# Kernel optimization log

Measured on AMD Instinct MI355X. Metric: run time of the kernel, lower is better.

## Reference

```python
import jax, jax.numpy as jnp
import numpy as np

CUTOFF = 8.0
NUM_G = 50
HID = 128
NUM_INTER = 3
NUM_NODES = 50000
NUM_EDGES = 1600000
NUM_GRAPHS = 128
MAX_Z = 100
LOG2 = float(np.log(2.0))


def ssp(x):
    # PyG ShiftedSoftplus
    return jax.nn.softplus(x) - LOG2


def setup_inputs() -> dict:
    key = jax.random.key(0)
    ks = jax.random.split(key, 20)
    s = 0.1
    pos = jax.random.normal(ks[0], (NUM_NODES, 3), dtype=jnp.float32) * 4.0
    edge_shift = jax.random.normal(ks[1], (NUM_EDGES, 3), dtype=jnp.float32) * 0.5
    z = jax.random.randint(ks[2], (NUM_NODES,), 0, MAX_Z, dtype=jnp.int32)
    edge_index = jax.random.randint(ks[3], (2, NUM_EDGES), 0, NUM_NODES, dtype=jnp.int32)
    batch = jnp.sort(jax.random.randint(ks[4], (NUM_NODES,), 0, NUM_GRAPHS, dtype=jnp.int32))
    emb = jax.random.normal(ks[5], (MAX_Z, HID), dtype=jnp.float32) * s
    mlp_w1 = jax.random.normal(ks[6], (NUM_INTER, NUM_G, HID), dtype=jnp.float32) * s
    mlp_b1 = jnp.zeros((NUM_INTER, HID), jnp.float32)
    mlp_w2 = jax.random.normal(ks[7], (NUM_INTER, HID, HID), dtype=jnp.float32) * s
    mlp_b2 = jnp.zeros((NUM_INTER, HID), jnp.float32)
    cf_w1 = jax.random.normal(ks[8], (NUM_INTER, HID, HID), dtype=jnp.float32) * s  # no bias (PyG lin1)
    cf_w2 = jax.random.normal(ks[9], (NUM_INTER, HID, HID), dtype=jnp.float32) * s
    cf_b2 = jnp.zeros((NUM_INTER, HID), jnp.float32)
    lin_w = jax.random.normal(ks[10], (NUM_INTER, HID, HID), dtype=jnp.float32) * s
    lin_b = jnp.zeros((NUM_INTER, HID), jnp.float32)
    head_w1 = jax.random.normal(ks[11], (HID, HID // 2), dtype=jnp.float32) * s
    head_b1 = jnp.zeros((HID // 2,), jnp.float32)
    head_w2 = jax.random.normal(ks[12], (HID // 2, 1), dtype=jnp.float32) * s
    head_b2 = jnp.zeros((1,), jnp.float32)
    return dict(pos=pos, edge_shift=edge_shift, emb=emb, mlp_w1=mlp_w1, mlp_b1=mlp_b1,
                mlp_w2=mlp_w2, mlp_b2=mlp_b2, cf_w1=cf_w1, cf_w2=cf_w2, cf_b2=cf_b2,
                lin_w=lin_w, lin_b=lin_b, head_w1=head_w1, head_b1=head_b1,
                head_w2=head_w2, head_b2=head_b2, z=z, edge_index=edge_index, batch=batch)


def reference(pos, edge_shift, emb, mlp_w1, mlp_b1, mlp_w2, mlp_b2, cf_w1, cf_w2, cf_b2,
              lin_w, lin_b, head_w1, head_b1, head_w2, head_b2, z, edge_index, batch):
    src, dst = edge_index[0], edge_index[1]
    # edge distances: pos[row] - (pos[col] + shift)
    rel = pos[src] - (pos[dst] + edge_shift)            # [E,3]
    w = jnp.linalg.norm(rel, axis=-1)                   # [E]
    # Gaussian smearing
    offset = jnp.linspace(0.0, CUTOFF, NUM_G, dtype=pos.dtype)
    coeff = -0.5 / (offset[1] - offset[0]) ** 2
    edge_attr = jnp.exp(coeff * (w[:, None] - offset) ** 2)   # [E,50]
    # cosine cutoff
    C = 0.5 * (jnp.cos(w * jnp.pi / CUTOFF) + 1.0)            # [E]
    h = emb[z]                                                # [N,128]
    for i in range(NUM_INTER):
        Wf = (ssp(edge_attr @ mlp_w1[i] + mlp_b1[i]) @ mlp_w2[i] + mlp_b2[i]) * C[:, None]  # [E,128]
        msg = (h @ cf_w1[i])[src] * Wf                   # gather-multiply  [E,128]
        agg = jax.ops.segment_sum(msg, dst, num_segments=NUM_NODES)         # scatter-sum [N,128]
        h = h + (ssp(agg @ cf_w2[i] + cf_b2[i]) @ lin_w[i] + lin_b[i])
    out_atom = ssp(h @ head_w1 + head_b1) @ head_w2 + head_b2               # [N,1]
    sums = jax.ops.segment_sum(out_atom, batch, num_segments=NUM_GRAPHS)    # [G,1]
    counts = jax.ops.segment_sum(jnp.ones((NUM_NODES, 1), out_atom.dtype), batch, num_segments=NUM_GRAPHS)
    return sums / jnp.maximum(counts, 1.0)  # mean readout; out_proj is Identity (128==128)
```

## Files before the change

kernel.cpp:

```cpp
#include <hip/hip_runtime.h>
#include <hip/hip_fp16.h>
#include <math.h>

#define NNODES  50000
#define NEDGES  1600000
#define NGRAPHS 128
#define HID     128
#define NG      50
#define NITER   3
#define TPTS    2048
#define WMAX    12.0f
#define PI_F    3.14159265358979323846f

__device__ __forceinline__ float ssp(float x) {
    float sp = fmaxf(x, 0.0f) + log1pf(expf(-fabsf(x)));
    return sp - 0.69314718055994530942f;
}

__global__ __launch_bounds__(256) void k_init_h(const float* __restrict__ emb,
                                                const int* __restrict__ z,
                                                float* __restrict__ h)
{
    int idx = blockIdx.x * 256 + threadIdx.x;
    int n = idx >> 7, c = idx & 127;
    h[idx] = emb[(z[n] << 7) + c];
}

__global__ __launch_bounds__(128) void k_table(const float* __restrict__ W1,
                                               const float* __restrict__ B1,
                                               const float* __restrict__ W2,
                                               const float* __restrict__ B2,
                                               float* __restrict__ table)
{
    int it = blockIdx.x / TPTS;
    int pt = blockIdx.x - it * TPTS;
    const float* W1i = W1 + (size_t)it * NG * HID;
    const float* B1i = B1 + (size_t)it * HID;
    const float* W2i = W2 + (size_t)it * HID * HID;
    const float* B2i = B2 + (size_t)it * HID;

    float w = pt * (WMAX / (float)(TPTS - 1));
    __shared__ float sEA[NG];
    __shared__ float sT1[HID];
    int k = threadIdx.x;
    if (k < NG) {
        float dx = 8.0f / 49.0f;
        float coeff = -0.5f / (dx * dx);
        float diff = w - (float)k * dx;
        sEA[k] = expf(coeff * diff * diff);
    }
    __syncthreads();
    float acc = B1i[k];
    for (int g = 0; g < NG; ++g) acc = fmaf(sEA[g], W1i[g * HID + k], acc);
    sT1[k] = ssp(acc);
    __syncthreads();
    float acc2 = B2i[k];
    for (int j = 0; j < HID; ++j) acc2 = fmaf(sT1[j], W2i[j * HID + k], acc2);
    table[(size_t)blockIdx.x * HID + k] = acc2;
}

__global__ __launch_bounds__(256) void k_tdelta(const float* __restrict__ raw,
                                                __half* __restrict__ ti)
{
    int idx = blockIdx.x * 256 + threadIdx.x;
    int c = idx & 127;
    int pt_it = idx >> 7;
    int pt = pt_it & (TPTS - 1);
    float v = raw[idx];
    float nv = (pt == TPTS - 1) ? v : raw[idx + HID];
    ti[(size_t)pt_it * 256 + c * 2]     = __float2half(v);
    ti[(size_t)pt_it * 256 + c * 2 + 1] = __float2half(nv - v);
}

__global__ __launch_bounds__(256) void k_hist(const int* __restrict__ ei,
                                              int* __restrict__ deg)
{
    int e = blockIdx.x * 256 + threadIdx.x;
    if (e >= NEDGES) return;
    atomicAdd(&deg[ei[NEDGES + e]], 1);
}

#define SCAN_T 1024
#define CHUNK  49
__global__ __launch_bounds__(SCAN_T) void k_scan(const int* __restrict__ deg,
                                                 int* __restrict__ rowptr,
                                                 int* __restrict__ cursor)
{
    int tid = threadIdx.x;
    int base = tid * CHUNK;
    int vals[CHUNK];
    int local = 0;
    #pragma unroll
    for (int i = 0; i < CHUNK; ++i) {
        int idx = base + i;
        int v = (idx < NNODES) ? deg[idx] : 0;
        vals[i] = local;
        local += v;
    }
    int lane = tid & 63, wid = tid >> 6;
    int x = local;
    #pragma unroll
    for (int off = 1; off < 64; off <<= 1) {
        int y = __shfl_up(x, off);
        if (lane >= off) x += y;
    }
    __shared__ int wsum[16];
    __shared__ int woff[17];
    if (lane == 63) wsum[wid] = x;
    __syncthreads();
    if (tid == 0) {
        int acc = 0;
        #pragma unroll
        for (int i = 0; i < 16; ++i) { woff[i] = acc; acc += wsum[i]; }
        woff[16] = acc;
    }
    __syncthreads();
    int threadExcl = woff[wid] + x - local;
    #pragma unroll
    for (int i = 0; i < CHUNK; ++i) {
        int idx = base + i;
        if (idx < NNODES) {
            int p = threadExcl + vals[i];
            rowptr[idx] = p;
            cursor[idx] = p;
        }
    }
    if (tid == SCAN_T - 1) rowptr[NNODES] = woff[16];
}

__global__ __launch_bounds__(256) void k_scatter(const int* __restrict__ ei,
                                                 const float* __restrict__ pos,
                                                 const float* __restrict__ shift,
                                                 int* __restrict__ cursor,
                                                 float2* __restrict__ rec)
{
    int e = blockIdx.x * 256 + threadIdx.x;
    if (e >= NEDGES) return;
    int s = ei[e], d = ei[NEDGES + e];
    float rx = pos[3*s+0] - (pos[3*d+0] + shift[3*e+0]);
    float ry = pos[3*s+1] - (pos[3*d+1] + shift[3*e+1]);
    float rz = pos[3*s+2] - (pos[3*d+2] + shift[3*e+2]);
    float w = sqrtf(rx*rx + ry*ry + rz*rz);
    int slot = atomicAdd(&cursor[d], 1);
    rec[slot] = make_float2(__int_as_float(s), w);
}

__device__ __forceinline__ void edge_contrib(float2 r, int lane,
                                             const __half2* __restrict__ hfH,
                                             const __half* __restrict__ tableH,
                                             float& ax, float& ay)
{
    int   s = __float_as_int(r.x);
    float w = r.y;
    const float SCALE = (float)(TPTS - 1) / WMAX;
    float t = fminf(w * SCALE, (float)(TPTS - 1));
    int i0 = (int)t; if (i0 > TPTS - 2) i0 = TPTS - 2;
    float fr = t - (float)i0;
    float C = 0.5f * (__cosf(w * (PI_F / 8.0f)) + 1.0f);
    uint2 tv = *((const uint2*)(tableH + (size_t)i0 * 256) + lane);
    __half2 hv = hfH[(size_t)s * 64 + lane];
    float2 p0 = __half22float2(*(__half2*)&tv.x);
    float2 p1 = __half22float2(*(__half2*)&tv.y);
    float2 hf2 = __half22float2(hv);
    ax = fmaf(fmaf(fr, p0.y, p0.x) * C, hf2.x, ax);
    ay = fmaf(fmaf(fr, p1.y, p1.x) * C, hf2.y, ay);
}

__global__ __launch_bounds__(256) void k_gather(const float2* __restrict__ rec,
                                                const int* __restrict__ rowptr,
                                                const __half2* __restrict__ hfH,
                                                const __half* __restrict__ tableH,
                                                float* __restrict__ agg)
{
    int node = blockIdx.x * 4 + (threadIdx.x >> 6);
    int lane = threadIdx.x & 63;
    int beg = rowptr[node], end = rowptr[node + 1];
    float ax0 = 0.f, ay0 = 0.f, ax1 = 0.f, ay1 = 0.f;
    int k = beg;
    for (; k + 4 <= end; k += 4) {
        float2 r0 = rec[k];
        float2 r1 = rec[k + 1];
        float2 r2 = rec[k + 2];
        float2 r3 = rec[k + 3];
        edge_contrib(r0, lane, hfH, tableH, ax0, ay0);
        edge_contrib(r1, lane, hfH, tableH, ax1, ay1);
        edge_contrib(r2, lane, hfH, tableH, ax0, ay0);
        edge_contrib(r3, lane, hfH, tableH, ax1, ay1);
    }
    for (; k < end; ++k) {
        float2 r0 = rec[k];
        edge_contrib(r0, lane, hfH, tableH, ax0, ay0);
    }
    *(float2*)(agg + (size_t)node * HID + lane * 2) = make_float2(ax0 + ax1, ay0 + ay1);
}

__global__ __launch_bounds__(512) void k_node_gemm(const float* __restrict__ A,
                                                   const float* __restrict__ W,
                                                   __half* __restrict__ outH)
{
    __shared__ float sA[128 * 132];
    int r0 = blockIdx.x * 128;
    int tid = threadIdx.x;
    for (int idx = tid; idx < 128 * 32; idx += 512) {
        int r = idx >> 5, c4 = idx & 31;
        int row = r0 + r;
        float4 v = make_float4(0.f, 0.f, 0.f, 0.f);
        if (row < NNODES) v = *(const float4*)(A + (size_t)row * HID + c4 * 4);
        *(float4*)(&sA[r * 132 + c4 * 4]) = v;
    }
    __syncthreads();
    int tx = tid & 15, ty = tid >> 4;
    int cc = tx * 8, ee = ty * 4;
    float acc[4][8];
    #pragma unroll
    for (int e = 0; e < 4; ++e)
        #pragma unroll
        for (int c = 0; c < 8; ++c) acc[e][c] = 0.f;
    for (int j = 0; j < HID; ++j) {
        float a[4];
        #pragma unroll
        for (int e = 0; e < 4; ++e) a[e] = sA[(ee + e) * 132 + j];
        float4 w0 = *(const float4*)(W + (size_t)j * HID + cc);
        float4 w1 = *(const float4*)(W + (size_t)j * HID + cc + 4);
        float wv[8] = {w0.x,w0.y,w0.z,w0.w,w1.x,w1.y,w1.z,w1.w};
        #pragma unroll
        for (int e = 0; e < 4; ++e)
            #pragma unroll
            for (int c = 0; c < 8; ++c)
                acc[e][c] = fmaf(a[e], wv[c], acc[e][c]);
    }
    #pragma unroll
    for (int e = 0; e < 4; ++e) {
        int row = r0 + ee + e;
        if (row < NNODES) {
            __half2 p0 = __floats2half2_rn(acc[e][0], acc[e][1]);
            __half2 p1 = __floats2half2_rn(acc[e][2], acc[e][3]);
            __half2 p2 = __floats2half2_rn(acc[e][4], acc[e][5]);
            __half2 p3 = __floats2half2_rn(acc[e][6], acc[e][7]);
            uint4 pk;
            pk.x = *(unsigned*)&p0; pk.y = *(unsigned*)&p1;
            pk.z = *(unsigned*)&p2; pk.w = *(unsigned*)&p3;
            *(uint4*)(outH + (size_t)row * HID + cc) = pk;
        }
    }
}

__global__ __launch_bounds__(512) void k_node_update(const float* __restrict__ agg,
                                                     const float* __restrict__ W,
                                                     const float* __restrict__ B,
                                                     const float* __restrict__ L,
                                                     const float* __restrict__ LB,
                                                     float* __restrict__ h)
{
    __shared__ float sA[128 * 132];
    int r0 = blockIdx.x * 128;
    int tid = threadIdx.x;
    for (int idx = tid; idx < 128 * 32; idx += 512) {
        int r = idx >> 5, c4 = idx & 31;
        int row = r0 + r;
        float4 v = make_float4(0.f, 0.f, 0.f, 0.f);
        if (row < NNODES) v = *(const float4*)(agg + (size_t)row * HID + c4 * 4);
        *(float4*)(&sA[r * 132 + c4 * 4]) = v;
    }
    __syncthreads();
    int tx = tid & 15, ty = tid >> 4;
    int cc = tx * 8, ee = ty * 4;
    float acc[4][8];
    {
        float4 b0 = *(const float4*)(B + cc);
        float4 b1 = *(const float4*)(B + cc + 4);
        #pragma unroll
        for (int e = 0; e < 4; ++e) {
            acc[e][0]=b0.x; acc[e][1]=b0.y; acc[e][2]=b0.z; acc[e][3]=b0.w;
            acc[e][4]=b1.x; acc[e][5]=b1.y; acc[e][6]=b1.z; acc[e][7]=b1.w;
        }
    }
    for (int j = 0; j < HID; ++j) {
        float a[4];
        #pragma unroll
        for (int e = 0; e < 4; ++e) a[e] = sA[(ee + e) * 132 + j];
        float4 w0 = *(const float4*)(W + (size_t)j * HID + cc);
        float4 w1 = *(const float4*)(W + (size_t)j * HID + cc + 4);
        float wv[8] = {w0.x,w0.y,w0.z,w0.w,w1.x,w1.y,w1.z,w1.w};
        #pragma unroll
        for (int e = 0; e < 4; ++e)
            #pragma unroll
            for (int c = 0; c < 8; ++c)
                acc[e][c] = fmaf(a[e], wv[c], acc[e][c]);
    }
    __syncthreads();
    #pragma unroll
    for (int e = 0; e < 4; ++e)
        #pragma unroll
        for (int c = 0; c < 8; ++c)
            sA[(ee + e) * 132 + cc + c] = ssp(acc[e][c]);
    __syncthreads();
    float acc2[4][8];
    {
        float4 b0 = *(const float4*)(LB + cc);
        float4 b1 = *(const float4*)(LB + cc + 4);
        #pragma unroll
        for (int e = 0; e < 4; ++e) {
            acc2[e][0]=b0.x; acc2[e][1]=b0.y; acc2[e][2]=b0.z; acc2[e][3]=b0.w;
            acc2[e][4]=b1.x; acc2[e][5]=b1.y; acc2[e][6]=b1.z; acc2[e][7]=b1.w;
        }
    }
    for (int j = 0; j < HID; ++j) {
        float a[4];
        #pragma unroll
        for (int e = 0; e < 4; ++e) a[e] = sA[(ee + e) * 132 + j];
        float4 w0 = *(const float4*)(L + (size_t)j * HID + cc);
        float4 w1 = *(const float4*)(L + (size_t)j * HID + cc + 4);
        float wv[8] = {w0.x,w0.y,w0.z,w0.w,w1.x,w1.y,w1.z,w1.w};
        #pragma unroll
        for (int e = 0; e < 4; ++e)
            #pragma unroll
            for (int c = 0; c < 8; ++c)
                acc2[e][c] = fmaf(a[e], wv[c], acc2[e][c]);
    }
    #pragma unroll
    for (int e = 0; e < 4; ++e) {
        int row = r0 + ee + e;
        if (row < NNODES) {
            float4* hp0 = (float4*)(h + (size_t)row * HID + cc);
            float4* hp1 = (float4*)(h + (size_t)row * HID + cc + 4);
            float4 h0 = *hp0, h1 = *hp1;
            h0.x += acc2[e][0]; h0.y += acc2[e][1]; h0.z += acc2[e][2]; h0.w += acc2[e][3];
            h1.x += acc2[e][4]; h1.y += acc2[e][5]; h1.z += acc2[e][6]; h1.w += acc2[e][7];
            *hp0 = h0; *hp1 = h1;
        }
    }
}

__global__ __launch_bounds__(512) void k_head(const float* __restrict__ h,
                                              const float* __restrict__ w1,
                                              const float* __restrict__ b1,
                                              const float* __restrict__ w2,
                                              const float* __restrict__ b2,
                                              const int* __restrict__ batch,
                                              float* __restrict__ sums_pad)
{
    __shared__ float sA[128 * 132];
    int r0 = blockIdx.x * 128;
    int tid = threadIdx.x;
    for (int idx = tid; idx < 128 * 32; idx += 512) {
        int r = idx >> 5, c4 = idx & 31;
        int row = r0 + r;
        float4 v = make_float4(0.f, 0.f, 0.f, 0.f);
        if (row < NNODES) v = *(const float4*)(h + (size_t)row * HID + c4 * 4);
        *(float4*)(&sA[r * 132 + c4 * 4]) = v;
    }
    __syncthreads();
    int tx = tid & 7, ty = tid >> 3;
    int cc = tx * 8, ee = ty * 2;
    float acc[2][8];
    {
        float4 b0 = *(const float4*)(b1 + cc);
        float4 bb = *(const float4*)(b1 + cc + 4);
        #pragma unroll
        for (int e = 0; e < 2; ++e) {
            acc[e][0]=b0.x; acc[e][1]=b0.y; acc[e][2]=b0.z; acc[e][3]=b0.w;
            acc[e][4]=bb.x; acc[e][5]=bb.y; acc[e][6]=bb.z; acc[e][7]=bb.w;
        }
    }
    #pragma unroll 4
    for (int j = 0; j < HID; ++j) {
        float a0 = sA[(ee + 0) * 132 + j];
        float a1 = sA[(ee + 1) * 132 + j];
        float4 w0 = *(const float4*)(w1 + (size_t)j * 64 + cc);
        float4 wv1 = *(const float4*)(w1 + (size_t)j * 64 + cc + 4);
        float wv[8] = {w0.x,w0.y,w0.z,w0.w,wv1.x,wv1.y,wv1.z,wv1.w};
        #pragma unroll
        for (int c = 0; c < 8; ++c) {
            acc[0][c] = fmaf(a0, wv[c], acc[0][c]);
            acc[1][c] = fmaf(a1, wv[c], acc[1][c]);
        }
    }
    float4 w2a = *(const float4*)(w2 + cc);
    float4 w2b = *(const float4*)(w2 + cc + 4);
    float w2v[8] = {w2a.x,w2a.y,w2a.z,w2a.w,w2b.x,w2b.y,w2b.z,w2b.w};
    float bias2 = b2[0];
    #pragma unroll
    for (int e = 0; e < 2; ++e) {
        float part = 0.f;
        #pragma unroll
        for (int c = 0; c < 8; ++c) part = fmaf(ssp(acc[e][c]), w2v[c], part);
        part += __shfl_down(part, 4, 8);
        part += __shfl_down(part, 2, 8);
        part += __shfl_down(part, 1, 8);
        if (tx == 0) {
            int row = r0 + ee + e;
            if (row < NNODES) {
                int b = batch[row];
                atomicAdd(&sums_pad[b * 16], part + bias2);
            }
        }
    }
}

__global__ void k_final(const float* __restrict__ sums_pad,
                        const int* __restrict__ batch,
                        float* __restrict__ out)
{
    int g = threadIdx.x;
    if (g >= NGRAPHS) return;
    int lo = 0, hi = NNODES;
    while (lo < hi) { int mid = (lo + hi) >> 1; if (batch[mid] < g) lo = mid + 1; else hi = mid; }
    int a = lo;
    lo = 0; hi = NNODES;
    while (lo < hi) { int mid = (lo + hi) >> 1; if (batch[mid] < g + 1) lo = mid + 1; else hi = mid; }
    float cnt = (float)(lo - a);
    out[g] = sums_pad[g * 16] / fmaxf(cnt, 1.0f);
}

extern "C" void kernel_launch(void* const* d_in, const int* in_sizes, int n_in,
                              void* d_out, int out_size, void* d_ws, size_t ws_size,
                              hipStream_t stream)
{
    const float* pos     = (const float*)d_in[0];
    const float* shift   = (const float*)d_in[1];
    const float* emb     = (const float*)d_in[2];
    const float* mlp_w1  = (const float*)d_in[3];
    const float* mlp_b1  = (const float*)d_in[4];
    const float* mlp_w2  = (const float*)d_in[5];
    const float* mlp_b2  = (const float*)d_in[6];
    const float* cf_w1   = (const float*)d_in[7];
    const float* cf_w2   = (const float*)d_in[8];
    const float* cf_b2   = (const float*)d_in[9];
    const float* lin_w   = (const float*)d_in[10];
    const float* lin_b   = (const float*)d_in[11];
    const float* head_w1 = (const float*)d_in[12];
    const float* head_b1 = (const float*)d_in[13];
    const float* head_w2 = (const float*)d_in[14];
    const float* head_b2 = (const float*)d_in[15];
    const int*   z       = (const int*)d_in[16];
    const int*   ei      = (const int*)d_in[17];
    const int*   batch   = (const int*)d_in[18];
    float* out = (float*)d_out;

    float* ws = (float*)d_ws;
    size_t off = 0;
    float*  h       = ws + off; off += (size_t)NNODES * HID;
    __half* hfH     = (__half*)(ws + off); off += (size_t)(NNODES + 48) * HID / 2;
    float*  agg     = ws + off; off += (size_t)NNODES * HID;
    float*  rawT    = ws + off; off += (size_t)3 * TPTS * HID;
    __half* tableH  = (__half*)(ws + off); off += (size_t)3 * TPTS * HID;
    float2* rec     = (float2*)(ws + off); off += (size_t)2 * NEDGES;
    int*    rowptr  = (int*)(ws + off); off += NNODES + 1;
    int*    deg     = (int*)(ws + off); off += NNODES;
    int*    cursor  = (int*)(ws + off); off += NNODES;
    float*  sums_pad= ws + off; off += NGRAPHS * 16;

    hipMemsetAsync(deg, 0, NNODES * sizeof(int), stream);
    hipMemsetAsync(sums_pad, 0, NGRAPHS * 16 * sizeof(float), stream);

    k_hist<<<(NEDGES + 255) / 256, 256, 0, stream>>>(ei, deg);
    k_scan<<<1, SCAN_T, 0, stream>>>(deg, rowptr, cursor);
    k_scatter<<<(NEDGES + 255) / 256, 256, 0, stream>>>(ei, pos, shift, cursor, rec);

    k_init_h<<<NNODES * HID / 256, 256, 0, stream>>>(emb, z, h);
    k_table<<<3 * TPTS, 128, 0, stream>>>(mlp_w1, mlp_b1, mlp_w2, mlp_b2, rawT);
    k_tdelta<<<(3 * TPTS * HID) / 256, 256, 0, stream>>>(rawT, tableH);

    int gblk = (NNODES + 127) / 128;
    for (int i = 0; i < NITER; ++i) {
        k_node_gemm<<<gblk, 512, 0, stream>>>(h, cf_w1 + (size_t)i * HID * HID, hfH);
        k_gather<<<NNODES / 4, 256, 0, stream>>>(rec, rowptr, (const __half2*)hfH,
                                                 tableH + (size_t)i * TPTS * HID * 2, agg);
        k_node_update<<<gblk, 512, 0, stream>>>(agg, cf_w2 + (size_t)i * HID * HID,
                                                cf_b2 + (size_t)i * HID,
                                                lin_w + (size_t)i * HID * HID,
                                                lin_b + (size_t)i * HID, h);
    }
    k_head<<<gblk, 512, 0, stream>>>(h, head_w1, head_b1, head_w2, head_b2, batch, sums_pad);
    k_final<<<1, 128, 0, stream>>>(sums_pad, batch, out);
}
```

Baseline: 1.077 ms.

## Move node GEMMs to fp16 MFMA with pre-transposed half weights

Replaces the fp32 SIMT tiled node GEMMs, both the cf_w1 projection and the fused cf_w2/ssp/lin update, with MFMA 16x16x16 fp16 kernels. Weights are transposed once into fp16, and h is kept in a second fp16 copy that the update kernel writes. The gather now stores agg as fp16, halving its write and read traffic. The intermediate ssp activations go through a swizzled LDS tile. This lowers the precision of the GEMM inputs and agg to fp16 and adds small setup kernels.

```diff
diff --git a/kernel.cpp b/kernel.cpp
--- a/kernel.cpp
+++ b/kernel.cpp
@@ -12,6 +12,9 @@
 #define WMAX    12.0f
 #define PI_F    3.14159265358979323846f
 
+typedef __attribute__((ext_vector_type(4))) _Float16 half4;
+typedef __attribute__((ext_vector_type(4))) float   f32x4;
+
 __device__ __forceinline__ float ssp(float x) {
     float sp = fmaxf(x, 0.0f) + log1pf(expf(-fabsf(x)));
     return sp - 0.69314718055994530942f;
@@ -19,11 +22,21 @@
 
 __global__ __launch_bounds__(256) void k_init_h(const float* __restrict__ emb,
                                                 const int* __restrict__ z,
-                                                float* __restrict__ h)
+                                                float* __restrict__ h,
+                                                _Float16* __restrict__ hH)
 {
     int idx = blockIdx.x * 256 + threadIdx.x;
     int n = idx >> 7, c = idx & 127;
-    h[idx] = emb[(z[n] << 7) + c];
+    float v = emb[(z[n] << 7) + c];
+    h[idx] = v;
+    hH[idx] = (_Float16)v;
+}
+
+__global__ __launch_bounds__(128) void k_wt(const float* __restrict__ in,
+                                            _Float16* __restrict__ out)
+{
+    int it = blockIdx.x >> 7, c = blockIdx.x & 127, j = threadIdx.x;
+    out[(size_t)it * 16384 + c * 128 + j] = (_Float16)in[(size_t)it * 16384 + j * 128 + c];
 }
 
 __global__ __launch_bounds__(128) void k_table(const float* __restrict__ W1,
@@ -170,7 +183,7 @@
                                                 const int* __restrict__ rowptr,
                                                 const __half2* __restrict__ hfH,
                                                 const __half* __restrict__ tableH,
-                                                float* __restrict__ agg)
+                                                __half2* __restrict__ aggH)
 {
     int node = blockIdx.x * 4 + (threadIdx.x >> 6);
     int lane = threadIdx.x & 63;
@@ -191,143 +204,106 @@
         float2 r0 = rec[k];
         edge_contrib(r0, lane, hfH, tableH, ax0, ay0);
     }
-    *(float2*)(agg + (size_t)node * HID + lane * 2) = make_float2(ax0 + ax1, ay0 + ay1);
-}
-
-__global__ __launch_bounds__(512) void k_node_gemm(const float* __restrict__ A,
-                                                   const float* __restrict__ W,
-                                                   __half* __restrict__ outH)
-{
-    __shared__ float sA[128 * 132];
-    int r0 = blockIdx.x * 128;
+    aggH[(size_t)node * 64 + lane] = __floats2half2_rn(ax0 + ax1, ay0 + ay1);
+}
+
+__global__ __launch_bounds__(256) void k_ngemm_mfma(const _Float16* __restrict__ hH,
+                                                    const _Float16* __restrict__ Wt,
+                                                    _Float16* __restrict__ outH)
+{
     int tid = threadIdx.x;
-    for (int idx = tid; idx < 128 * 32; idx += 512) {
-        int r = idx >> 5, c4 = idx & 31;
-        int row = r0 + r;
-        float4 v = make_float4(0.f, 0.f, 0.f, 0.f);
-        if (row < NNODES) v = *(const float4*)(A + (size_t)row * HID + c4 * 4);
-        *(float4*)(&sA[r * 132 + c4 * 4]) = v;
-    }
-    __syncthreads();
-    int tx = tid & 15, ty = tid >> 4;
-    int cc = tx * 8, ee = ty * 4;
-    float acc[4][8];
-    #pragma unroll
-    for (int e = 0; e < 4; ++e)
-        #pragma unroll
-        for (int c = 0; c < 8; ++c) acc[e][c] = 0.f;
-    for (int j = 0; j < HID; ++j) {
-        float a[4];
-        #pragma unroll
-        for (int e = 0; e < 4; ++e) a[e] = sA[(ee + e) * 132 + j];
-        float4 w0 = *(const float4*)(W + (size_t)j * HID + cc);
-        float4 w1 = *(const float4*)(W + (size_t)j * HID + cc + 4);
-        float wv[8] = {w0.x,w0.y,w0.z,w0.w,w1.x,w1.y,w1.z,w1.w};
-        #pragma unroll
-        for (int e = 0; e < 4; ++e)
-            #pragma unroll
-            for (int c = 0; c < 8; ++c)
-                acc[e][c] = fmaf(a[e], wv[c], acc[e][c]);
-    }
-    #pragma unroll
-    for (int e = 0; e < 4; ++e) {
-        int row = r0 + ee + e;
-        if (row < NNODES) {
-            __half2 p0 = __floats2half2_rn(acc[e][0], acc[e][1]);
-            __half2 p1 = __floats2half2_rn(acc[e][2], acc[e][3]);
-            __half2 p2 = __floats2half2_rn(acc[e][4], acc[e][5]);
-            __half2 p3 = __floats2half2_rn(acc[e][6], acc[e][7]);
-            uint4 pk;
-            pk.x = *(unsigned*)&p0; pk.y = *(unsigned*)&p1;
-            pk.z = *(unsigned*)&p2; pk.w = *(unsigned*)&p3;
-            *(uint4*)(outH + (size_t)row * HID + cc) = pk;
-        }
-    }
-}
-
-__global__ __launch_bounds__(512) void k_node_update(const float* __restrict__ agg,
-                                                     const float* __restrict__ W,
-                                                     const float* __restrict__ B,
-                                                     const float* __restrict__ L,
+    int wave = tid >> 6, l = tid & 63;
+    int lr = l & 15, lg = l >> 4;
+    int r0 = blockIdx.x * 64 + wave * 16;
+    f32x4 acc[8];
+    #pragma unroll
+    for (int ct = 0; ct < 8; ++ct) acc[ct] = (f32x4){0.f, 0.f, 0.f, 0.f};
+    const _Float16* aRow = hH + (size_t)(r0 + lr) * HID;
+    #pragma unroll
+    for (int kk = 0; kk < 8; ++kk) {
+        half4 a = *(const half4*)(aRow + kk * 16 + lg * 4);
+        #pragma unroll
+        for (int ct = 0; ct < 8; ++ct) {
+            half4 b = *(const half4*)(Wt + (size_t)(ct * 16 + lr) * HID + kk * 16 + lg * 4);
+            acc[ct] = __builtin_amdgcn_mfma_f32_16x16x16f16(a, b, acc[ct], 0, 0, 0);
+        }
+    }
+    #pragma unroll
+    for (int ct = 0; ct < 8; ++ct) {
+        #pragma unroll
+        for (int r = 0; r < 4; ++r) {
+            int row = r0 + lg * 4 + r;
+            if (row < NNODES) outH[(size_t)row * HID + ct * 16 + lr] = (_Float16)acc[ct][r];
+        }
+    }
+}
+
+__global__ __launch_bounds__(256) void k_update_mfma(const _Float16* __restrict__ aggH,
+                                                     const _Float16* __restrict__ W2t,
+                                                     const float* __restrict__ B2,
+                                                     const _Float16* __restrict__ Lt,
                                                      const float* __restrict__ LB,
-                                                     float* __restrict__ h)
-{
-    __shared__ float sA[128 * 132];
-    int r0 = blockIdx.x * 128;
+                                                     float* __restrict__ h,
+                                                     _Float16* __restrict__ hH)
+{
+    __shared__ _Float16 sT[64 * 128];
     int tid = threadIdx.x;
-    for (int idx = tid; idx < 128 * 32; idx += 512) {
-        int r = idx >> 5, c4 = idx & 31;
-        int row = r0 + r;
-        float4 v = make_float4(0.f, 0.f, 0.f, 0.f);
-        if (row < NNODES) v = *(const float4*)(agg + (size_t)row * HID + c4 * 4);
-        *(float4*)(&sA[r * 132 + c4 * 4]) = v;
-    }
-    __syncthreads();
-    int tx = tid & 15, ty = tid >> 4;
-    int cc = tx * 8, ee = ty * 4;
-    float acc[4][8];
-    {
-        float4 b0 = *(const float4*)(B + cc);
-        float4 b1 = *(const float4*)(B + cc + 4);
-        #pragma unroll
-        for (int e = 0; e < 4; ++e) {
-            acc[e][0]=b0.x; acc[e][1]=b0.y; acc[e][2]=b0.z; acc[e][3]=b0.w;
-            acc[e][4]=b1.x; acc[e][5]=b1.y; acc[e][6]=b1.z; acc[e][7]=b1.w;
-        }
-    }
-    for (int j = 0; j < HID; ++j) {
-        float a[4];
-        #pragma unroll
-        for (int e = 0; e < 4; ++e) a[e] = sA[(ee + e) * 132 + j];
-        float4 w0 = *(const float4*)(W + (size_t)j * HID + cc);
-        float4 w1 = *(const float4*)(W + (size_t)j * HID + cc + 4);
-        float wv[8] = {w0.x,w0.y,w0.z,w0.w,w1.x,w1.y,w1.z,w1.w};
-        #pragma unroll
-        for (int e = 0; e < 4; ++e)
-            #pragma unroll
-            for (int c = 0; c < 8; ++c)
-                acc[e][c] = fmaf(a[e], wv[c], acc[e][c]);
-    }
-    __syncthreads();
-    #pragma unroll
-    for (int e = 0; e < 4; ++e)
-        #pragma unroll
-        for (int c = 0; c < 8; ++c)
-            sA[(ee + e) * 132 + cc + c] = ssp(acc[e][c]);
-    __syncthreads();
-    float acc2[4][8];
-    {
-        float4 b0 = *(const float4*)(LB + cc);
-        float4 b1 = *(const float4*)(LB + cc + 4);
-        #pragma unroll
-        for (int e = 0; e < 4; ++e) {
-            acc2[e][0]=b0.x; acc2[e][1]=b0.y; acc2[e][2]=b0.z; acc2[e][3]=b0.w;
-            acc2[e][4]=b1.x; acc2[e][5]=b1.y; acc2[e][6]=b1.z; acc2[e][7]=b1.w;
-        }
-    }
-    for (int j = 0; j < HID; ++j) {
-        float a[4];
-        #pragma unroll
-        for (int e = 0; e < 4; ++e) a[e] = sA[(ee + e) * 132 + j];
-        float4 w0 = *(const float4*)(L + (size_t)j * HID + cc);
-        float4 w1 = *(const float4*)(L + (size_t)j * HID + cc + 4);
-        float wv[8] = {w0.x,w0.y,w0.z,w0.w,w1.x,w1.y,w1.z,w1.w};
-        #pragma unroll
-        for (int e = 0; e < 4; ++e)
-            #pragma unroll
-            for (int c = 0; c < 8; ++c)
-                acc2[e][c] = fmaf(a[e], wv[c], acc2[e][c]);
-    }
-    #pragma unroll
-    for (int e = 0; e < 4; ++e) {
-        int row = r0 + ee + e;
-        if (row < NNODES) {
-            float4* hp0 = (float4*)(h + (size_t)row * HID + cc);
-            float4* hp1 = (float4*)(h + (size_t)row * HID + cc + 4);
-            float4 h0 = *hp0, h1 = *hp1;
-            h0.x += acc2[e][0]; h0.y += acc2[e][1]; h0.z += acc2[e][2]; h0.w += acc2[e][3];
-            h1.x += acc2[e][4]; h1.y += acc2[e][5]; h1.z += acc2[e][6]; h1.w += acc2[e][7];
-            *hp0 = h0; *hp1 = h1;
+    int wave = tid >> 6, l = tid & 63;
+    int lr = l & 15, lg = l >> 4;
+    int r0 = blockIdx.x * 64 + wave * 16;
+
+    f32x4 acc[8];
+    #pragma unroll
+    for (int ct = 0; ct < 8; ++ct) acc[ct] = (f32x4){0.f, 0.f, 0.f, 0.f};
+    const _Float16* aRow = aggH + (size_t)(r0 + lr) * HID;
+    #pragma unroll
+    for (int kk = 0; kk < 8; ++kk) {
+        half4 a = *(const half4*)(aRow + kk * 16 + lg * 4);
+        #pragma unroll
+        for (int ct = 0; ct < 8; ++ct) {
+            half4 b = *(const half4*)(W2t + (size_t)(ct * 16 + lr) * HID + kk * 16 + lg * 4);
+            acc[ct] = __builtin_amdgcn_mfma_f32_16x16x16f16(a, b, acc[ct], 0, 0, 0);
+        }
+    }
+    #pragma unroll
+    for (int ct = 0; ct < 8; ++ct) {
+        #pragma unroll
+        for (int r = 0; r < 4; ++r) {
+            int rl = wave * 16 + lg * 4 + r;
+            int col = ct * 16 + lr;
+            float v = ssp(acc[ct][r] + B2[col]);
+            int byte = rl * 256 + col * 2;
+            byte ^= (rl & 7) << 4;
+            *(_Float16*)((char*)sT + byte) = (_Float16)v;
+        }
+    }
+    __syncthreads();
+    f32x4 acc2[8];
+    #pragma unroll
+    for (int ct = 0; ct < 8; ++ct) acc2[ct] = (f32x4){0.f, 0.f, 0.f, 0.f};
+    int rl2 = wave * 16 + lr;
+    #pragma unroll
+    for (int kk = 0; kk < 8; ++kk) {
+        int byte = rl2 * 256 + (kk * 16 + lg * 4) * 2;
+        byte ^= (rl2 & 7) << 4;
+        half4 a = *(const half4*)((char*)sT + byte);
+        #pragma unroll
+        for (int ct = 0; ct < 8; ++ct) {
+            half4 b = *(const half4*)(Lt + (size_t)(ct * 16 + lr) * HID + kk * 16 + lg * 4);
+            acc2[ct] = __builtin_amdgcn_mfma_f32_16x16x16f16(a, b, acc2[ct], 0, 0, 0);
+        }
+    }
+    #pragma unroll
+    for (int ct = 0; ct < 8; ++ct) {
+        #pragma unroll
+        for (int r = 0; r < 4; ++r) {
+            int row = r0 + lg * 4 + r;
+            int col = ct * 16 + lr;
+            if (row < NNODES) {
+                float hv = h[(size_t)row * HID + col] + acc2[ct][r] + LB[col];
+                h[(size_t)row * HID + col] = hv;
+                hH[(size_t)row * HID + col] = (_Float16)hv;
+            }
         }
     }
 }
@@ -440,16 +416,20 @@
 
     float* ws = (float*)d_ws;
     size_t off = 0;
-    float*  h       = ws + off; off += (size_t)NNODES * HID;
-    __half* hfH     = (__half*)(ws + off); off += (size_t)(NNODES + 48) * HID / 2;
-    float*  agg     = ws + off; off += (size_t)NNODES * HID;
-    float*  rawT    = ws + off; off += (size_t)3 * TPTS * HID;
-    __half* tableH  = (__half*)(ws + off); off += (size_t)3 * TPTS * HID;
-    float2* rec     = (float2*)(ws + off); off += (size_t)2 * NEDGES;
-    int*    rowptr  = (int*)(ws + off); off += NNODES + 1;
-    int*    deg     = (int*)(ws + off); off += NNODES;
-    int*    cursor  = (int*)(ws + off); off += NNODES;
-    float*  sums_pad= ws + off; off += NGRAPHS * 16;
+    float*    h       = ws + off; off += (size_t)NNODES * HID;
+    _Float16* hH      = (_Float16*)(ws + off); off += (size_t)(NNODES + 64) * HID / 2;
+    _Float16* hfH     = (_Float16*)(ws + off); off += (size_t)(NNODES + 64) * HID / 2;
+    _Float16* aggH    = (_Float16*)(ws + off); off += (size_t)(NNODES + 64) * HID / 2;
+    float*    rawT    = ws + off; off += (size_t)3 * TPTS * HID;
+    __half*   tableH  = (__half*)(ws + off); off += (size_t)3 * TPTS * HID;
+    _Float16* w1t     = (_Float16*)(ws + off); off += (size_t)3 * HID * HID / 2;
+    _Float16* w2t     = (_Float16*)(ws + off); off += (size_t)3 * HID * HID / 2;
+    _Float16* lwt     = (_Float16*)(ws + off); off += (size_t)3 * HID * HID / 2;
+    float2*   rec     = (float2*)(ws + off); off += (size_t)2 * NEDGES;
+    int*      rowptr  = (int*)(ws + off); off += NNODES + 1;
+    int*      deg     = (int*)(ws + off); off += NNODES;
+    int*      cursor  = (int*)(ws + off); off += NNODES;
+    float*    sums_pad= ws + off; off += NGRAPHS * 16;
 
     hipMemsetAsync(deg, 0, NNODES * sizeof(int), stream);
     hipMemsetAsync(sums_pad, 0, NGRAPHS * 16 * sizeof(float), stream);
@@ -458,20 +438,24 @@
     k_scan<<<1, SCAN_T, 0, stream>>>(deg, rowptr, cursor);
     k_scatter<<<(NEDGES + 255) / 256, 256, 0, stream>>>(ei, pos, shift, cursor, rec);
 
-    k_init_h<<<NNODES * HID / 256, 256, 0, stream>>>(emb, z, h);
+    k_init_h<<<NNODES * HID / 256, 256, 0, stream>>>(emb, z, h, hH);
     k_table<<<3 * TPTS, 128, 0, stream>>>(mlp_w1, mlp_b1, mlp_w2, mlp_b2, rawT);
     k_tdelta<<<(3 * TPTS * HID) / 256, 256, 0, stream>>>(rawT, tableH);
-
-    int gblk = (NNODES + 127) / 128;
+    k_wt<<<3 * 128, 128, 0, stream>>>(cf_w1, w1t);
+    k_wt<<<3 * 128, 128, 0, stream>>>(cf_w2, w2t);
+    k_wt<<<3 * 128, 128, 0, stream>>>(lin_w, lwt);
+
+    int gblk = (NNODES + 63) / 64;
     for (int i = 0; i < NITER; ++i) {
-        k_node_gemm<<<gblk, 512, 0, stream>>>(h, cf_w1 + (size_t)i * HID * HID, hfH);
+        k_ngemm_mfma<<<gblk, 256, 0, stream>>>(hH, w1t + (size_t)i * HID * HID, hfH);
         k_gather<<<NNODES / 4, 256, 0, stream>>>(rec, rowptr, (const __half2*)hfH,
-                                                 tableH + (size_t)i * TPTS * HID * 2, agg);
-        k_node_update<<<gblk, 512, 0, stream>>>(agg, cf_w2 + (size_t)i * HID * HID,
+                                                 tableH + (size_t)i * TPTS * HID * 2,
+                                                 (__half2*)aggH);
+        k_update_mfma<<<gblk, 256, 0, stream>>>(aggH, w2t + (size_t)i * HID * HID,
                                                 cf_b2 + (size_t)i * HID,
-                                                lin_w + (size_t)i * HID * HID,
-                                                lin_b + (size_t)i * HID, h);
-    }
-    k_head<<<gblk, 512, 0, stream>>>(h, head_w1, head_b1, head_w2, head_b2, batch, sums_pad);
+                                                lwt + (size_t)i * HID * HID,
+                                                lin_b + (size_t)i * HID, h, hH);
+    }
+    k_head<<<(NNODES + 127) / 128, 512, 0, stream>>>(h, head_w1, head_b1, head_w2, head_b2, batch, sums_pad);
     k_final<<<1, 128, 0, stream>>>(sums_pad, batch, out);
 }
```

Result: faster. 1.051 ms (-2.4%).
